# Kernel optimization log

Measured on AMD Instinct MI355X. Metric: run time of the kernel, lower is better.

## Reference

```python
import jax, jax.numpy as jnp
import numpy as np


def setup_inputs() -> dict:
    key = jax.random.key(0)
    ks = jax.random.split(key, 5)
    B, S, H = 4, 4096, 512
    std = 1.0 / np.sqrt(H)
    x = jax.random.normal(ks[0], (B, S, H), dtype=jnp.float32)
    relative_pos = jax.random.normal(ks[1], (B, S, H), dtype=jnp.float32)
    Wq = jax.random.normal(ks[2], (H, H), dtype=jnp.float32) * std
    Wk = jax.random.normal(ks[3], (H, H), dtype=jnp.float32) * std
    Wv = jax.random.normal(ks[4], (H, H), dtype=jnp.float32) * std
    bq = jnp.zeros((H,), dtype=jnp.float32)
    bk = jnp.zeros((H,), dtype=jnp.float32)
    bv = jnp.zeros((H,), dtype=jnp.float32)
    return {"x": x, "relative_pos": relative_pos, "Wq": Wq, "bq": bq,
            "Wk": Wk, "bk": bk, "Wv": Wv, "bv": bv}


def reference(x, relative_pos, Wq, bq, Wk, bk, Wv, bv):
    H = x.shape[-1]
    scale = jnp.sqrt(jnp.asarray(H, dtype=x.dtype))
    # torch Linear: y = x @ W^T + b
    Q = jnp.einsum('bsh,oh->bso', x, Wq) + bq
    K = jnp.einsum('bsh,oh->bso', x, Wk) + bk
    V = jnp.einsum('bsh,oh->bso', x, Wv) + bv
    Kr = jnp.einsum('bsh,oh->bso', relative_pos, Wk) + bk
    # two score terms, each [B,S,S]
    scores = (jnp.einsum('bqd,bkd->bqk', Q, K) +
              jnp.einsum('bqd,bkd->bqk', Q, Kr)) / scale
    weights = jax.nn.softmax(scores, axis=-1)
    return jnp.einsum('bqk,bkd->bqd', weights, V)
```

## Files before the change

kernel.cpp:

```cpp
#include <hip/hip_runtime.h>
#include <stdint.h>

typedef __attribute__((ext_vector_type(8))) short bf16x8;
typedef __attribute__((ext_vector_type(4))) float f32x4;

#define AS1 __attribute__((address_space(1)))
#define AS3 __attribute__((address_space(3)))

__device__ __forceinline__ void gl2lds16(const void* g, void* l) {
    __builtin_amdgcn_global_load_lds((const AS1 void*)g, (AS3 void*)l, 16, 0, 0);
}

__device__ __forceinline__ unsigned short f2bf(float f) {
    uint32_t u = __builtin_bit_cast(uint32_t, f);
    uint32_t r = (u + 0x7fffu + ((u >> 16) & 1u)) >> 16;
    return (unsigned short)r;
}

constexpr int S = 4096;
constexpr int H = 512;
constexpr size_t OFF_XB  = 0;
constexpr size_t OFF_SB  = 16777216;
constexpr size_t OFF_WQB = 33554432;
constexpr size_t OFF_WKB = 34078720;
constexpr size_t OFF_WVB = 34603008;
constexpr size_t OFF_BQK = 35127296;
constexpr size_t OFF_QB  = 35131392;
constexpr size_t OFF_K2B = OFF_QB  + 16777216;
constexpr size_t OFF_VTB = OFF_K2B + 16777216;
constexpr size_t OFF_PB  = OFF_VTB + 16777216;
constexpr size_t OFF_L   = OFF_PB  + 134217728;

__global__ __launch_bounds__(256) void prep_all(const float* __restrict__ x,
                                                const float* __restrict__ rp,
                                                const float* __restrict__ wq,
                                                const float* __restrict__ wk,
                                                const float* __restrict__ wv,
                                                const float* __restrict__ bq,
                                                const float* __restrict__ bk,
                                                unsigned short* __restrict__ xb,
                                                unsigned short* __restrict__ sb,
                                                unsigned short* __restrict__ wqb,
                                                unsigned short* __restrict__ wkb,
                                                unsigned short* __restrict__ wvb,
                                                float* __restrict__ bqk,
                                                float* __restrict__ lrow) {
    if (blockIdx.x < 8192) {
        const int i = (blockIdx.x * 256 + threadIdx.x) * 4;
        float4 xv = *(const float4*)(x + i);
        float4 rv = *(const float4*)(rp + i);
        uint2 xo, so;
        xo.x = (uint32_t)f2bf(xv.x) | ((uint32_t)f2bf(xv.y) << 16);
        xo.y = (uint32_t)f2bf(xv.z) | ((uint32_t)f2bf(xv.w) << 16);
        so.x = (uint32_t)f2bf(xv.x + rv.x) | ((uint32_t)f2bf(xv.y + rv.y) << 16);
        so.y = (uint32_t)f2bf(xv.z + rv.z) | ((uint32_t)f2bf(xv.w + rv.w) << 16);
        *(uint2*)(xb + i) = xo;
        *(uint2*)(sb + i) = so;
    } else {
        const int t = (blockIdx.x - 8192) * 256 + threadIdx.x;
        const int i = t * 4;
        float4 q = *(const float4*)(wq + i);
        float4 k = *(const float4*)(wk + i);
        float4 v = *(const float4*)(wv + i);
        uint2 o;
        o.x = (uint32_t)f2bf(q.x) | ((uint32_t)f2bf(q.y) << 16);
        o.y = (uint32_t)f2bf(q.z) | ((uint32_t)f2bf(q.w) << 16);
        *(uint2*)(wqb + i) = o;
        o.x = (uint32_t)f2bf(k.x) | ((uint32_t)f2bf(k.y) << 16);
        o.y = (uint32_t)f2bf(k.z) | ((uint32_t)f2bf(k.w) << 16);
        *(uint2*)(wkb + i) = o;
        o.x = (uint32_t)f2bf(v.x) | ((uint32_t)f2bf(v.y) << 16);
        o.y = (uint32_t)f2bf(v.z) | ((uint32_t)f2bf(v.w) << 16);
        *(uint2*)(wvb + i) = o;
        if (t < 128) {
            *(float4*)(bqk + t * 4) = *(const float4*)(bq + t * 4);
        } else if (t < 256) {
            const int u = t - 128;
            float4 b = *(const float4*)(bk + u * 4);
            *(float4*)(bqk + 512 + u * 4) = make_float4(2.f * b.x, 2.f * b.y, 2.f * b.z, 2.f * b.w);
        }
        if (t < 4096) {
            *(float4*)(lrow + t * 4) = make_float4(0.f, 0.f, 0.f, 0.f);
        }
    }
}

template <int MODE, int SWZ, int NPANEL>
__global__ __launch_bounds__(256, 2)
void gemm_bt(const unsigned short* __restrict__ Abase,
             const unsigned short* __restrict__ Bbase,
             void* __restrict__ Cbase,
             int M, int N, int K,
             long long sAz, long long sBz, long long sCz,
             const float* __restrict__ bias_n, long long sBNz,
             const float* __restrict__ bias_m,
             float scale,
             float* __restrict__ rowdiv, long long sRz)
{
    int bx = blockIdx.x, by = blockIdx.y, bz = blockIdx.z;
    if (SWZ) {
        const int gx = gridDim.x, gy = gridDim.y;
        const int id  = bx + gx * (by + gridDim.y * bz);
        const int xcd = id & 7;
        const int k   = id >> 3;
        const int kg  = k / gx;
        bx = k - kg * gx;
        const int g = xcd + 8 * kg;
        const int gz = g / gy;
        by = g - gz * gy;
        bz = gz;
    }
    const int z = bz;
    const unsigned short* A  = Abase + (size_t)z * (size_t)sAz;
    const unsigned short* Bm = Bbase + (size_t)z * (size_t)sBz;
    const int bn = bx * 128;
    const int bm = by * 128;

    constexpr int STAGE_BYTES = NPANEL * 16384;
    constexpr int SMEM_BYTES = (MODE == 1) ? STAGE_BYTES
                             : (STAGE_BYTES > 34816 ? STAGE_BYTES : 34816);
    __shared__ __align__(16) char smem[SMEM_BYTES];
    unsigned short* As = (unsigned short*)smem;
    unsigned short* Bs = (unsigned short*)(smem + NPANEL * 8192);

    const int tid  = threadIdx.x;
    const int wave = tid >> 6;
    const int lane = tid & 63;
    const int lm   = lane & 15;
    const int quad = lane >> 4;
    const int wm   = (wave >> 1) * 64;
    const int wn   = (wave & 1) * 64;

    const int r0 = tid >> 2;
    const int p0 = tid & 3;

    f32x4 acc[4][4] = {};

    for (int k0 = 0; k0 < K; k0 += 32 * NPANEL) {
        __syncthreads();
        #pragma unroll
        for (int pp = 0; pp < NPANEL; pp++) {
            const unsigned short* Ap = A  + (size_t)(bm + r0) * K + k0 + pp * 32 + p0 * 8;
            const unsigned short* Bp = Bm + (size_t)(bn + r0) * K + k0 + pp * 32 + p0 * 8;
            unsigned short* Asp = As + pp * 4096;
            unsigned short* Bsp = Bs + pp * 4096;
            gl2lds16(Ap,                    Asp + wave * 512);
            gl2lds16(Ap + (size_t)64 * K,   Asp + 2048 + wave * 512);
            gl2lds16(Bp,                    Bsp + wave * 512);
            gl2lds16(Bp + (size_t)64 * K,   Bsp + 2048 + wave * 512);
        }
        __syncthreads();

        #pragma unroll
        for (int pp = 0; pp < NPANEL; pp++) {
            bf16x8 af[4], bfr[4];
            #pragma unroll
            for (int t = 0; t < 4; t++)
                af[t]  = *(const bf16x8*)(As + pp * 4096 + (wm + t * 16 + lm) * 32 + quad * 8);
            #pragma unroll
            for (int t = 0; t < 4; t++)
                bfr[t] = *(const bf16x8*)(Bs + pp * 4096 + (wn + t * 16 + lm) * 32 + quad * 8);
            #pragma unroll
            for (int mt = 0; mt < 4; mt++)
                #pragma unroll
                for (int nt = 0; nt < 4; nt++)
                    acc[mt][nt] = __builtin_amdgcn_mfma_f32_16x16x32_bf16(af[mt], bfr[nt], acc[mt][nt], 0, 0, 0);
        }
    }

    if (MODE == 1) {
        float* C = (float*)Cbase + (size_t)z * (size_t)sCz;
        const float* rd = rowdiv + (size_t)z * (size_t)sRz;
        #pragma unroll
        for (int mt = 0; mt < 4; mt++) {
            #pragma unroll
            for (int i = 0; i < 4; i++) {
                const int row = bm + wm + mt * 16 + quad * 4 + i;
                const float inv = 1.0f / rd[row];
                const size_t rb = (size_t)row * (size_t)N;
                #pragma unroll
                for (int nt = 0; nt < 4; nt++) {
                    const int col = bn + wn + nt * 16 + lm;
                    C[rb + col] = acc[mt][nt][i] * inv;
                }
            }
        }
    } else {
        unsigned short* C = (unsigned short*)Cbase + (size_t)z * (size_t)sCz;
        const float* bn_ptr = (MODE == 0 && bias_n) ? bias_n + (size_t)z * (size_t)sBNz : nullptr;
        float* lr = (MODE == 2) ? rowdiv + (size_t)z * (size_t)sRz : nullptr;
        unsigned short* Ct = (unsigned short*)smem;
        __syncthreads();
        #pragma unroll
        for (int mt = 0; mt < 4; mt++) {
            #pragma unroll
            for (int i = 0; i < 4; i++) {
                const int r = wm + mt * 16 + quad * 4 + i;
                if (MODE == 0) {
                    const float badd = bias_m ? bias_m[bm + r] : 0.0f;
                    #pragma unroll
                    for (int nt = 0; nt < 4; nt++) {
                        const int col = bn + wn + nt * 16 + lm;
                        float v = acc[mt][nt][i] * scale + badd;
                        if (bn_ptr) v += bn_ptr[col];
                        Ct[r * 136 + wn + nt * 16 + lm] = f2bf(v);
                    }
                } else {
                    float rsum = 0.f;
                    #pragma unroll
                    for (int nt = 0; nt < 4; nt++) {
                        float p = __expf(acc[mt][nt][i] * scale);
                        rsum += p;
                        Ct[r * 136 + wn + nt * 16 + lm] = f2bf(p);
                    }
                    rsum += __shfl_xor(rsum, 1);
                    rsum += __shfl_xor(rsum, 2);
                    rsum += __shfl_xor(rsum, 4);
                    rsum += __shfl_xor(rsum, 8);
                    if (lm == 0) atomicAdd(lr + bm + r, rsum);
                }
            }
        }
        __syncthreads();
        #pragma unroll
        for (int j = 0; j < 8; j++) {
            const int r   = (tid >> 4) + 16 * j;
            const int c16 = tid & 15;
            uint4 vv = *(const uint4*)(Ct + r * 136 + c16 * 8);
            *(uint4*)(C + (size_t)(bm + r) * (size_t)N + bn + c16 * 8) = vv;
        }
    }
}

extern "C" void kernel_launch(void* const* d_in, const int* in_sizes, int n_in,
                              void* d_out, int out_size, void* d_ws, size_t ws_size,
                              hipStream_t stream) {
    const float* x  = (const float*)d_in[0];
    const float* rp = (const float*)d_in[1];
    const float* Wq = (const float*)d_in[2];
    const float* bq = (const float*)d_in[3];
    const float* Wk = (const float*)d_in[4];
    const float* bk = (const float*)d_in[5];
    const float* Wv = (const float*)d_in[6];
    const float* bv = (const float*)d_in[7];

    char* ws = (char*)d_ws;
    unsigned short* xb  = (unsigned short*)(ws + OFF_XB);
    unsigned short* sb  = (unsigned short*)(ws + OFF_SB);
    unsigned short* wqb = (unsigned short*)(ws + OFF_WQB);
    unsigned short* wkb = (unsigned short*)(ws + OFF_WKB);
    unsigned short* wvb = (unsigned short*)(ws + OFF_WVB);
    float*          bqk = (float*)(ws + OFF_BQK);
    unsigned short* qb  = (unsigned short*)(ws + OFF_QB);
    unsigned short* k2b = (unsigned short*)(ws + OFF_K2B);
    unsigned short* vtb = (unsigned short*)(ws + OFF_VTB);
    unsigned short* pb  = (unsigned short*)(ws + OFF_PB);
    float*          lrow = (float*)(ws + OFF_L);

    prep_all<<<8448, 256, 0, stream>>>(x, rp, Wq, Wk, Wv, bq, bk,
                                       xb, sb, wqb, wkb, wvb, bqk, lrow);

    gemm_bt<0, 1, 2><<<dim3(4, 128, 2), 256, 0, stream>>>(
        xb, wqb, qb, 16384, 512, 512,
        8388608, 262144, 8388608,
        bqk, 512, nullptr, 1.0f, nullptr, 0);
    gemm_bt<0, 0, 2><<<dim3(32, 4, 4), 256, 0, stream>>>(
        wvb, xb, vtb, 512, 4096, 512,
        0, (long long)S * H, (long long)S * H,
        nullptr, 0, bv, 1.0f, nullptr, 0);
    gemm_bt<2, 0, 2><<<dim3(32, 32, 4), 256, 0, stream>>>(
        qb, k2b, pb, 4096, 4096, 512,
        (long long)S * H, (long long)S * H, (long long)S * S,
        nullptr, 0, nullptr, 0.044194173824159216f,
        lrow, 4096);
    gemm_bt<1, 1, 4><<<dim3(4, 32, 4), 256, 0, stream>>>(
        pb, vtb, d_out, 4096, 512, 4096,
        (long long)S * S, (long long)S * H, (long long)S * H,
        nullptr, 0, nullptr, 1.0f, lrow, 4096);
}
```

Before: 342.9 us.

## Split-K the P·V GEMM with atomic accumulation and drop LDS row padding

The final P·V GEMM is split into two K halves, which doubles the grid from 512 to 1024 blocks. Partial results are accumulated into the zeroed output with float atomicAdd, and a memset is added up front. The panel count per stage drops from 4 to 2. The epilogue LDS staging stride also changes from 136 to 128, removing the padding. The aim is better occupancy and load balance on the final GEMM, at the cost of atomic traffic, an extra memset, and possible LDS bank conflicts on the unpadded stores.

```diff
diff --git a/kernel.cpp b/kernel.cpp
--- a/kernel.cpp
+++ b/kernel.cpp
@@ -85,12 +85,12 @@
     }
 }
 
-template <int MODE, int SWZ, int NPANEL>
+template <int MODE, int SWZ, int NPANEL, int SPLITK>
 __global__ __launch_bounds__(256, 2)
 void gemm_bt(const unsigned short* __restrict__ Abase,
              const unsigned short* __restrict__ Bbase,
              void* __restrict__ Cbase,
-             int M, int N, int K,
+             int M, int N, int K, int LD,
              long long sAz, long long sBz, long long sCz,
              const float* __restrict__ bias_n, long long sBNz,
              const float* __restrict__ bias_m,
@@ -110,15 +110,16 @@
         by = g - gz * gy;
         bz = gz;
     }
-    const int z = bz;
-    const unsigned short* A  = Abase + (size_t)z * (size_t)sAz;
-    const unsigned short* Bm = Bbase + (size_t)z * (size_t)sBz;
+    const int z    = SPLITK ? (bz >> 1) : bz;
+    const long long koff = SPLITK ? (long long)(bz & 1) * K : 0;
+    const unsigned short* A  = Abase + (size_t)z * (size_t)sAz + koff;
+    const unsigned short* Bm = Bbase + (size_t)z * (size_t)sBz + koff;
     const int bn = bx * 128;
     const int bm = by * 128;
 
     constexpr int STAGE_BYTES = NPANEL * 16384;
-    constexpr int SMEM_BYTES = (MODE == 1) ? STAGE_BYTES
-                             : (STAGE_BYTES > 34816 ? STAGE_BYTES : 34816);
+    constexpr int SMEM_BYTES = (MODE == 1 || MODE == 3) ? STAGE_BYTES
+                             : (STAGE_BYTES > 32768 ? STAGE_BYTES : 32768);
     __shared__ __align__(16) char smem[SMEM_BYTES];
     unsigned short* As = (unsigned short*)smem;
     unsigned short* Bs = (unsigned short*)(smem + NPANEL * 8192);
@@ -140,14 +141,14 @@
         __syncthreads();
         #pragma unroll
         for (int pp = 0; pp < NPANEL; pp++) {
-            const unsigned short* Ap = A  + (size_t)(bm + r0) * K + k0 + pp * 32 + p0 * 8;
-            const unsigned short* Bp = Bm + (size_t)(bn + r0) * K + k0 + pp * 32 + p0 * 8;
+            const unsigned short* Ap = A  + (size_t)(bm + r0) * LD + k0 + pp * 32 + p0 * 8;
+            const unsigned short* Bp = Bm + (size_t)(bn + r0) * LD + k0 + pp * 32 + p0 * 8;
             unsigned short* Asp = As + pp * 4096;
             unsigned short* Bsp = Bs + pp * 4096;
             gl2lds16(Ap,                    Asp + wave * 512);
-            gl2lds16(Ap + (size_t)64 * K,   Asp + 2048 + wave * 512);
+            gl2lds16(Ap + (size_t)64 * LD,  Asp + 2048 + wave * 512);
             gl2lds16(Bp,                    Bsp + wave * 512);
-            gl2lds16(Bp + (size_t)64 * K,   Bsp + 2048 + wave * 512);
+            gl2lds16(Bp + (size_t)64 * LD,  Bsp + 2048 + wave * 512);
         }
         __syncthreads();
 
@@ -168,7 +169,7 @@
         }
     }
 
-    if (MODE == 1) {
+    if (MODE == 1 || MODE == 3) {
         float* C = (float*)Cbase + (size_t)z * (size_t)sCz;
         const float* rd = rowdiv + (size_t)z * (size_t)sRz;
         #pragma unroll
@@ -181,7 +182,8 @@
                 #pragma unroll
                 for (int nt = 0; nt < 4; nt++) {
                     const int col = bn + wn + nt * 16 + lm;
-                    C[rb + col] = acc[mt][nt][i] * inv;
+                    if (MODE == 1) C[rb + col] = acc[mt][nt][i] * inv;
+                    else           atomicAdd(C + rb + col, acc[mt][nt][i] * inv);
                 }
             }
         }
@@ -203,7 +205,7 @@
                         const int col = bn + wn + nt * 16 + lm;
                         float v = acc[mt][nt][i] * scale + badd;
                         if (bn_ptr) v += bn_ptr[col];
-                        Ct[r * 136 + wn + nt * 16 + lm] = f2bf(v);
+                        Ct[r * 128 + wn + nt * 16 + lm] = f2bf(v);
                     }
                 } else {
                     float rsum = 0.f;
@@ -211,7 +213,7 @@
                     for (int nt = 0; nt < 4; nt++) {
                         float p = __expf(acc[mt][nt][i] * scale);
                         rsum += p;
-                        Ct[r * 136 + wn + nt * 16 + lm] = f2bf(p);
+                        Ct[r * 128 + wn + nt * 16 + lm] = f2bf(p);
                     }
                     rsum += __shfl_xor(rsum, 1);
                     rsum += __shfl_xor(rsum, 2);
@@ -226,7 +228,7 @@
         for (int j = 0; j < 8; j++) {
             const int r   = (tid >> 4) + 16 * j;
             const int c16 = tid & 15;
-            uint4 vv = *(const uint4*)(Ct + r * 136 + c16 * 8);
+            uint4 vv = *(const uint4*)(Ct + r * 128 + c16 * 8);
             *(uint4*)(C + (size_t)(bm + r) * (size_t)N + bn + c16 * 8) = vv;
         }
     }
@@ -257,24 +259,26 @@
     unsigned short* pb  = (unsigned short*)(ws + OFF_PB);
     float*          lrow = (float*)(ws + OFF_L);
 
+    hipMemsetAsync(d_out, 0, (size_t)out_size * sizeof(float), stream);
+
     prep_all<<<8448, 256, 0, stream>>>(x, rp, Wq, Wk, Wv, bq, bk,
                                        xb, sb, wqb, wkb, wvb, bqk, lrow);
 
-    gemm_bt<0, 1, 2><<<dim3(4, 128, 2), 256, 0, stream>>>(
-        xb, wqb, qb, 16384, 512, 512,
+    gemm_bt<0, 1, 2, 0><<<dim3(4, 128, 2), 256, 0, stream>>>(
+        xb, wqb, qb, 16384, 512, 512, 512,
         8388608, 262144, 8388608,
         bqk, 512, nullptr, 1.0f, nullptr, 0);
-    gemm_bt<0, 0, 2><<<dim3(32, 4, 4), 256, 0, stream>>>(
-        wvb, xb, vtb, 512, 4096, 512,
+    gemm_bt<0, 0, 2, 0><<<dim3(32, 4, 4), 256, 0, stream>>>(
+        wvb, xb, vtb, 512, 4096, 512, 512,
         0, (long long)S * H, (long long)S * H,
         nullptr, 0, bv, 1.0f, nullptr, 0);
-    gemm_bt<2, 0, 2><<<dim3(32, 32, 4), 256, 0, stream>>>(
-        qb, k2b, pb, 4096, 4096, 512,
+    gemm_bt<2, 0, 2, 0><<<dim3(32, 32, 4), 256, 0, stream>>>(
+        qb, k2b, pb, 4096, 4096, 512, 512,
         (long long)S * H, (long long)S * H, (long long)S * S,
         nullptr, 0, nullptr, 0.044194173824159216f,
         lrow, 4096);
-    gemm_bt<1, 1, 4><<<dim3(4, 32, 4), 256, 0, stream>>>(
-        pb, vtb, d_out, 4096, 512, 4096,
+    gemm_bt<3, 1, 2, 1><<<dim3(4, 32, 8), 256, 0, stream>>>(
+        pb, vtb, d_out, 4096, 512, 2048, 4096,
         (long long)S * S, (long long)S * H, (long long)S * H,
         nullptr, 0, nullptr, 1.0f, lrow, 4096);
 }
```

After: 383.6 us. +11.9%, slower.
